# Performance work log

Measured on AMD Instinct MI355X. Metric: run time of the kernel, lower is better.

## Reference

```python
import jax, jax.numpy as jnp
import numpy as np

N = 100000   # nodes
E = 1600000  # edges
D = 128      # input_dim
H = 128      # hidden_dim
G = 64       # graphs in batch
L = 3        # num GCN layers
BN_EPS = 1e-5


def setup_inputs() -> dict:
    key = jax.random.key(0)
    ks = jax.random.split(key, 16)
    s = 1.0 / np.sqrt(H)
    inp = {
        "x": jax.random.normal(ks[0], (N, D), jnp.float32),
        "edge_index": jax.random.randint(ks[1], (2, E), 0, N, dtype=jnp.int64),
        "batch": jnp.sort(jax.random.randint(ks[2], (N,), 0, G, dtype=jnp.int64)),
        # stacked GCNConv params (input_dim == hidden_dim so layer 0 stacks too)
        "conv_w": jax.random.normal(ks[3], (L, H, H), jnp.float32) * s,
        "conv_b": jax.random.normal(ks[4], (L, H), jnp.float32) * 0.01,
        # BatchNorm1d running stats + affine (eval mode)
        "bn_gamma": jnp.ones((L, H), jnp.float32),
        "bn_beta": jnp.zeros((L, H), jnp.float32),
        "bn_mean": jax.random.normal(ks[5], (L, H), jnp.float32) * 0.1,
        "bn_var": jax.random.uniform(ks[6], (L, H), jnp.float32, 0.5, 1.5),
        # node head MLP
        "node_w1": jax.random.normal(ks[7], (H // 2, H), jnp.float32) * s,
        "node_b1": jnp.zeros((H // 2,), jnp.float32),
        "node_w2": jax.random.normal(ks[8], (2, H // 2), jnp.float32) * (1.0 / np.sqrt(H // 2)),
        "node_b2": jnp.zeros((2,), jnp.float32),
        # graph head MLP
        "graph_w1": jax.random.normal(ks[9], (H // 2, H), jnp.float32) * s,
        "graph_b1": jnp.zeros((H // 2,), jnp.float32),
        "graph_w2": jax.random.normal(ks[10], (2, H // 2), jnp.float32) * (1.0 / np.sqrt(H // 2)),
        "graph_b2": jnp.zeros((2,), jnp.float32),
    }
    return inp


def _gcn_layer(h, src, dst, deg_inv_sqrt, w, b):
    # PyG GCNConv: h' = W h, then symmetric-normalized scatter-add over
    # edges (self-loops already appended to src/dst).
    h = h @ w.T                                   # [N, H]
    norm = deg_inv_sqrt[src] * deg_inv_sqrt[dst]  # [E+N]
    msg = h[src] * norm[:, None]                  # [E+N, H] gather
    out = jax.ops.segment_sum(msg, dst, num_segments=N)  # scatter-add
    return out + b


def _forward(x, edge_index, batch, conv_w, conv_b, bn_gamma, bn_beta,
             bn_mean, bn_var, node_w1, node_b1, node_w2, node_b2,
             graph_w1, graph_b1, graph_w2, graph_b2):
    loops = jnp.arange(N, dtype=edge_index.dtype)
    src = jnp.concatenate([edge_index[0], loops])
    dst = jnp.concatenate([edge_index[1], loops])
    deg = jax.ops.segment_sum(jnp.ones_like(src, dtype=x.dtype), dst,
                              num_segments=N)
    deg_inv_sqrt = jnp.where(deg > 0, jax.lax.rsqrt(deg), 0.0)

    h = x
    for i in range(L):  # conv -> BN(eval) -> ReLU (dropout inactive in eval)
        h = _gcn_layer(h, src, dst, deg_inv_sqrt, conv_w[i], conv_b[i])
        h = (h - bn_mean[i]) * jax.lax.rsqrt(bn_var[i] + BN_EPS) * bn_gamma[i] + bn_beta[i]
        h = jax.nn.relu(h)

    node_pred = jax.nn.relu(h @ node_w1.T + node_b1) @ node_w2.T + node_b2

    counts = jax.ops.segment_sum(jnp.ones((N,), h.dtype), batch,
                                 num_segments=G)
    graph_emb = jax.ops.segment_sum(h, batch, num_segments=G) / \
        jnp.maximum(counts, 1.0)[:, None]
    graph_pred = jax.nn.relu(graph_emb @ graph_w1.T + graph_b1) @ graph_w2.T + graph_b2
    return node_pred, graph_pred


def reference(x, edge_index, batch, conv_w, conv_b, bn_gamma, bn_beta,
              bn_mean, bn_var, node_w1, node_b1, node_w2, node_b2,
              graph_w1, graph_b1, graph_w2, graph_b2):
    return _forward(x, edge_index, batch, conv_w, conv_b, bn_gamma, bn_beta,
                    bn_mean, bn_var, node_w1, node_b1, node_w2, node_b2,
                    graph_w1, graph_b1, graph_w2, graph_b2)
```

## Files before the change

### kernel.cpp

```cpp
#include <hip/hip_runtime.h>
#include <hip/hip_bf16.h>

#define NN 100000
#define EE 1600000
#define HH 128
#define GG 64
#define LL 3
#define BN_EPS 1e-5f
#define NT 391
#define CHW 392
#define CAP 6144

typedef __hip_bfloat16 bf16;
typedef __attribute__((ext_vector_type(8))) short short8;
typedef __attribute__((ext_vector_type(4))) float floatx4;

__device__ __forceinline__ float lo16(unsigned v) { return __uint_as_float(v << 16); }
__device__ __forceinline__ float hi16(unsigned v) { return __uint_as_float(v & 0xffff0000u); }
__device__ __forceinline__ unsigned short f2b(float v) {
    bf16 h = __float2bfloat16(v);
    return *(unsigned short*)&h;
}
__device__ __forceinline__ unsigned pack2(float a, float b) {
    return (unsigned)f2b(a) | ((unsigned)f2b(b) << 16);
}
__device__ __forceinline__ int geti(const int* __restrict__ p, int i, int f) {
    return f ? p[2 * i] : p[i];
}

__global__ __launch_bounds__(1024) void k_part(const int* __restrict__ ei,
        unsigned* __restrict__ chunk, unsigned short* __restrict__ lbu,
        int* __restrict__ flag,
        const float* __restrict__ conv_w, const float* __restrict__ nw1,
        unsigned short* __restrict__ cwB, unsigned short* __restrict__ n1B,
        float* __restrict__ bnA, float* __restrict__ bnB,
        const float* __restrict__ conv_b, const float* __restrict__ g,
        const float* __restrict__ be, const float* __restrict__ mn,
        const float* __restrict__ vr, float* __restrict__ gsum,
        float* __restrict__ gcnt) {
    __shared__ int lcnt[NT];
    __shared__ int sd[512];
    __shared__ unsigned short lbs[CHW];
    __shared__ unsigned sorted[4096];
    int t = threadIdx.x;
    int e0 = blockIdx.x * 4096;
    int probe = ei[2 * (e0 + (t & 63)) + 1];
    int f = __any(probe != 0) ? 0 : 1;
    if (blockIdx.x == 0 && t == 0) *flag = f;
    int gi = blockIdx.x * 1024 + t;
    if (gi < LL * HH * HH) cwB[gi] = f2b(conv_w[gi]);
    if (gi < 64 * HH) n1B[gi] = f2b(nw1[gi]);
    if (gi < LL * HH) {
        float A = g[gi] * rsqrtf(vr[gi] + BN_EPS);
        bnA[gi] = A;
        bnB[gi] = (conv_b[gi] - mn[gi]) * A + be[gi];
    }
    if (gi < GG * HH) gsum[gi] = 0.f;
    if (gi < GG) gcnt[gi] = 0.f;
    int nume = EE - e0 < 4096 ? EE - e0 : 4096;
    for (int i = t; i < NT; i += 1024) lcnt[i] = 0;
    __syncthreads();
    unsigned pk[4]; int ml[4], mt[4];
#pragma unroll
    for (int i = 0; i < 4; i++) {
        int li = i * 1024 + t;
        if (li < nume) {
            int e = e0 + li;
            int src = geti(ei, e, f), dst = geti(ei, EE + e, f);
            mt[i] = dst >> 8;
            pk[i] = ((unsigned)src << 8) | (unsigned)(dst & 255);
            ml[i] = atomicAdd(&lcnt[mt[i]], 1);
        }
    }
    __syncthreads();
    int own = 0;
    if (t < 512) {
        own = t < NT ? lcnt[t] : 0;
        sd[t] = own;
    }
    __syncthreads();
    for (int off = 1; off < 512; off <<= 1) {
        int y = 0;
        if (t < 512 && t >= off) y = sd[t - off];
        __syncthreads();
        if (t < 512) sd[t] += y;
        __syncthreads();
    }
    if (t < NT) lbs[t] = (unsigned short)(sd[t] - own);
    if (t == 0) lbs[NT] = (unsigned short)nume;
    __syncthreads();
#pragma unroll
    for (int i = 0; i < 4; i++) {
        int li = i * 1024 + t;
        if (li < nume) sorted[(int)lbs[mt[i]] + ml[i]] = pk[i];
    }
    if (t < CHW) lbu[blockIdx.x * CHW + t] = lbs[t];
    __syncthreads();
    for (int idx = t; idx < nume; idx += 1024)
        __builtin_nontemporal_store(sorted[idx], &chunk[e0 + idx]);
}

__global__ __launch_bounds__(1024) void k_csr(const unsigned* __restrict__ chunk,
        const unsigned short* __restrict__ lbu, unsigned* __restrict__ csr,
        int* __restrict__ offs, int* __restrict__ cnt, float* __restrict__ dinv,
        int* __restrict__ tne) {
    __shared__ unsigned stage[CAP];
    __shared__ unsigned outb[CAP];
    __shared__ int sd[512];
    __shared__ int hist[256], exs[256], cur[256];
    int T = blockIdx.x, t = threadIdx.x;
    int st = 0, rl = 0;
    if (t < NT) {
        int s0 = lbu[t * CHW + T];
        int s1 = lbu[t * CHW + T + 1];
        st = t * 4096 + s0;
        rl = s1 - s0;
    }
    if (t < 512) sd[t] = rl;
    __syncthreads();
    for (int off = 1; off < 512; off <<= 1) {
        int y = 0;
        if (t < 512 && t >= off) y = sd[t - off];
        __syncthreads();
        if (t < 512) sd[t] += y;
        __syncthreads();
    }
    int ne = sd[511];
    if (ne > CAP) ne = CAP;
    int so = t < NT ? sd[t] - rl : 0;
    if (t < 256) hist[t] = 0;
    __syncthreads();
    if (t < NT) {
        for (int j = 0; j < rl; j++) {
            int p = so + j;
            if (p < CAP)
                stage[p] = __builtin_nontemporal_load(&chunk[st + j]);
        }
    }
    __syncthreads();
    for (int i = t; i < ne; i += 1024)
        atomicAdd(&hist[stage[i] & 255u], 1);
    __syncthreads();
    int c = 0;
    if (t < 256) {
        c = hist[t];
        exs[t] = c;
    }
    __syncthreads();
    for (int off = 1; off < 256; off <<= 1) {
        int a = 0;
        if (t < 256 && t >= off) a = exs[t - off];
        __syncthreads();
        if (t < 256) exs[t] += a;
        __syncthreads();
    }
    if (t < 256) {
        int ex = exs[t] - c;
        cur[t] = ex;
        int node = T * 256 + t;
        if (node < NN) {
            offs[node] = T * CAP + ex;
            cnt[node] = c;
            dinv[node] = rsqrtf(1.0f + (float)c);
        }
    }
    if (t == 0) tne[T] = ne;
    __syncthreads();
    for (int i = t; i < ne; i += 1024) {
        unsigned p = stage[i];
        int q = atomicAdd(&cur[p & 255u], 1);
        outb[q] = p >> 8;
    }
    __syncthreads();
    for (int i = t; i < ne; i += 1024)
        csr[(size_t)T * CAP + i] = outb[i];
}

__global__ __launch_bounds__(1024) void k_wpack(const unsigned* __restrict__ csr,
        const float* __restrict__ dinv, unsigned* __restrict__ ewp,
        const int* __restrict__ tne) {
    int T = blockIdx.x, t = threadIdx.x;
    int ne = tne[T];
    for (int i = t; i < ne; i += 1024) {
        unsigned s = csr[(size_t)T * CAP + i];
        ewp[(size_t)T * CAP + i] = (s << 15) | ((unsigned)f2b(dinv[s]) & 0x7fffu);
    }
}

template<typename AT, int NC, bool FUSE>
__global__ __launch_bounds__(256) void k_gemm(const AT* __restrict__ in,
        const unsigned short* __restrict__ Wb, const float* __restrict__ bias,
        unsigned short* __restrict__ outh, int do_relu,
        const float* __restrict__ w2, const float* __restrict__ b2v,
        float* __restrict__ out2f) {
    int wave = threadIdx.x >> 6, lane = threadIdx.x & 63;
    int ln = lane & 15, q = lane >> 4;
    int r0 = blockIdx.x * 64 + wave * 16;
    int row = r0 + ln;
    int rr = row < NN ? row : NN - 1;
    short8 a[4];
    if constexpr (sizeof(AT) == 2) {
        const short8* ap = (const short8*)(in + (size_t)rr * HH);
#pragma unroll
        for (int kt = 0; kt < 4; kt++) a[kt] = ap[kt * 4 + q];
    } else {
        const float4* ap = (const float4*)(in + (size_t)rr * HH);
#pragma unroll
        for (int kt = 0; kt < 4; kt++) {
            float4 f0 = ap[(kt * 4 + q) * 2];
            float4 f1 = ap[(kt * 4 + q) * 2 + 1];
            a[kt][0] = (short)f2b(f0.x); a[kt][1] = (short)f2b(f0.y);
            a[kt][2] = (short)f2b(f0.z); a[kt][3] = (short)f2b(f0.w);
            a[kt][4] = (short)f2b(f1.x); a[kt][5] = (short)f2b(f1.y);
            a[kt][6] = (short)f2b(f1.z); a[kt][7] = (short)f2b(f1.w);
        }
    }
    float p0[4], p1[4];
    if constexpr (FUSE) {
#pragma unroll
        for (int r = 0; r < 4; r++) { p0[r] = 0.f; p1[r] = 0.f; }
    }
#pragma unroll
    for (int ct = 0; ct < NC / 16; ct++) {
        int c = ct * 16 + ln;
        const short8* bp = (const short8*)(Wb + (size_t)c * HH);
        floatx4 acc = {0.f, 0.f, 0.f, 0.f};
#pragma unroll
        for (int kt = 0; kt < 4; kt++) {
            short8 b = bp[kt * 4 + q];
            acc = __builtin_amdgcn_mfma_f32_16x16x32_bf16(a[kt], b, acc, 0, 0, 0);
        }
        float bv = bias ? bias[c] : 0.f;
        if constexpr (FUSE) {
            float wa = w2[c], wb = w2[64 + c];
#pragma unroll
            for (int reg = 0; reg < 4; reg++) {
                float v = fmaxf(acc[reg] + bv, 0.f);
                p0[reg] = fmaf(v, wa, p0[reg]);
                p1[reg] = fmaf(v, wb, p1[reg]);
            }
        } else {
#pragma unroll
            for (int reg = 0; reg < 4; reg++) {
                int orow = r0 + q * 4 + reg;
                if (orow < NN) {
                    float v = acc[reg] + bv;
                    if (do_relu) v = fmaxf(v, 0.f);
                    outh[(size_t)orow * NC + c] = f2b(v);
                }
            }
        }
    }
    if constexpr (FUSE) {
#pragma unroll
        for (int off = 1; off < 16; off <<= 1) {
#pragma unroll
            for (int r = 0; r < 4; r++) {
                p0[r] += __shfl_xor(p0[r], off);
                p1[r] += __shfl_xor(p1[r], off);
            }
        }
        if (ln == 0) {
            float ba = b2v[0], bb = b2v[1];
#pragma unroll
            for (int reg = 0; reg < 4; reg++) {
                int orow = r0 + q * 4 + reg;
                if (orow < NN)
                    ((float2*)out2f)[orow] = make_float2(p0[reg] + ba, p1[reg] + bb);
            }
        }
    }
}

__global__ __launch_bounds__(256) void k_aggr(const uint2* __restrict__ tH2,
        const unsigned* __restrict__ ewp, const int* __restrict__ offs,
        const int* __restrict__ cnt, const float* __restrict__ dinv,
        const float* __restrict__ bnA, const float* __restrict__ bnB,
        uint2* __restrict__ hout) {
    int wave = threadIdx.x >> 6, lane = threadIdx.x & 63;
    int node = blockIdx.x * 4 + wave;
    if (node >= NN) return;
    int base = offs[node], ne = cnt[node];
    float dd = dinv[node];
    int half = lane >> 5, li = lane & 31;
    uint2 sv = tH2[(size_t)node * 32 + li];
    float ws = half ? 0.f : dd;
    float4 acc;
    acc.x = lo16(sv.x) * ws; acc.y = hi16(sv.x) * ws;
    acc.z = lo16(sv.y) * ws; acc.w = hi16(sv.y) * ws;
    for (int k0 = 0; k0 < ne; k0 += 64) {
        int idx = k0 + lane;
        unsigned m = idx < ne ? __builtin_nontemporal_load(&ewp[base + idx]) : 0u;
        int c2 = ne - k0 < 64 ? ne - k0 : 64;
        for (int kk = 0; kk < c2; kk += 16) {
            uint2 vv[8]; float wj[8];
#pragma unroll
            for (int j = 0; j < 8; j++) {
                int e = kk + 2 * j + half;
                unsigned mm = (unsigned)__shfl((int)m, e);
                int s = (int)(mm >> 15);
                wj[j] = __uint_as_float((mm & 0x7fffu) << 16);
                vv[j] = tH2[(size_t)s * 32 + li];
            }
#pragma unroll
            for (int j = 0; j < 8; j++) {
                acc.x = fmaf(lo16(vv[j].x), wj[j], acc.x);
                acc.y = fmaf(hi16(vv[j].x), wj[j], acc.y);
                acc.z = fmaf(lo16(vv[j].y), wj[j], acc.z);
                acc.w = fmaf(hi16(vv[j].y), wj[j], acc.w);
            }
        }
    }
    acc.x += __shfl_xor(acc.x, 32);
    acc.y += __shfl_xor(acc.y, 32);
    acc.z += __shfl_xor(acc.z, 32);
    acc.w += __shfl_xor(acc.w, 32);
    if (half == 0) {
        float4 Av = ((const float4*)bnA)[li];
        float4 Bv = ((const float4*)bnB)[li];
        float r0 = fmaxf(fmaf(acc.x * dd, Av.x, Bv.x), 0.f);
        float r1 = fmaxf(fmaf(acc.y * dd, Av.y, Bv.y), 0.f);
        float r2 = fmaxf(fmaf(acc.z * dd, Av.z, Bv.z), 0.f);
        float r3 = fmaxf(fmaf(acc.w * dd, Av.w, Bv.w), 0.f);
        unsigned long long v64 =
            ((unsigned long long)pack2(r2, r3) << 32) | pack2(r0, r1);
        __builtin_nontemporal_store(v64,
            (unsigned long long*)&hout[(size_t)node * 32 + li]);
    }
}

#define PN 32
__global__ __launch_bounds__(64) void k_pool(const unsigned* __restrict__ hb,
        const int* __restrict__ batch, float* __restrict__ gsum,
        float* __restrict__ gcnt, const int* __restrict__ flag) {
    int lane = threadIdx.x;
    int f = *flag;
    int s0 = blockIdx.x * PN;
    int e0 = s0 + PN < NN ? s0 + PN : NN;
    int cur = geti(batch, s0, f);
    float a0 = 0.f, a1 = 0.f, cn = 0.f;
    for (int n = s0; n < e0; n++) {
        int g = geti(batch, n, f);
        if (g != cur) {
            atomicAdd(&gsum[cur * HH + 2 * lane], a0);
            atomicAdd(&gsum[cur * HH + 2 * lane + 1], a1);
            if (lane == 0) atomicAdd(&gcnt[cur], cn);
            a0 = a1 = cn = 0.f; cur = g;
        }
        unsigned v = hb[(size_t)n * 64 + lane];
        a0 += lo16(v); a1 += hi16(v); cn += 1.f;
    }
    atomicAdd(&gsum[cur * HH + 2 * lane], a0);
    atomicAdd(&gsum[cur * HH + 2 * lane + 1], a1);
    if (lane == 0) atomicAdd(&gcnt[cur], cn);
}

__global__ __launch_bounds__(64) void k_ghead(const float* __restrict__ gsum,
        const float* __restrict__ gcnt, const float* __restrict__ w1,
        const float* __restrict__ b1, const float* __restrict__ w2,
        const float* __restrict__ b2v, float* __restrict__ out) {
    __shared__ float emb[HH];
    int g = blockIdx.x, lane = threadIdx.x;
    float cn = gcnt[g];
    cn = cn > 1.f ? cn : 1.f;
    float inv = 1.f / cn;
    emb[lane] = gsum[g * HH + lane] * inv;
    emb[lane + 64] = gsum[g * HH + 64 + lane] * inv;
    __syncthreads();
    float acc = b1[lane];
    for (int k = 0; k < HH; k++) acc = fmaf(emb[k], w1[lane * HH + k], acc);
    float y = fmaxf(acc, 0.f);
    float v0 = y * w2[lane];
    float v1 = y * w2[64 + lane];
#pragma unroll
    for (int off = 32; off; off >>= 1) {
        v0 += __shfl_xor(v0, off);
        v1 += __shfl_xor(v1, off);
    }
    if (lane == 0) {
        out[(size_t)NN * 2 + g * 2]     = v0 + b2v[0];
        out[(size_t)NN * 2 + g * 2 + 1] = v1 + b2v[1];
    }
}

extern "C" void kernel_launch(void* const* d_in, const int* in_sizes, int n_in,
                              void* d_out, int out_size, void* d_ws, size_t ws_size,
                              hipStream_t stream) {
    const float* x      = (const float*)d_in[0];
    const int*   ei     = (const int*)d_in[1];
    const int*   batch  = (const int*)d_in[2];
    const float* conv_w = (const float*)d_in[3];
    const float* conv_b = (const float*)d_in[4];
    const float* bn_g   = (const float*)d_in[5];
    const float* bn_b   = (const float*)d_in[6];
    const float* bn_m   = (const float*)d_in[7];
    const float* bn_v   = (const float*)d_in[8];
    const float* nw1    = (const float*)d_in[9];
    const float* nb1    = (const float*)d_in[10];
    const float* nw2    = (const float*)d_in[11];
    const float* nb2    = (const float*)d_in[12];
    const float* gw1    = (const float*)d_in[13];
    const float* gb1    = (const float*)d_in[14];
    const float* gw2    = (const float*)d_in[15];
    const float* gb2    = (const float*)d_in[16];
    float* out = (float*)d_out;

    char* ws = (char*)d_ws;
    size_t off = 0;
    auto alloc = [&](size_t bytes) -> void* {
        void* p = ws + off;
        off += (bytes + 255) & ~(size_t)255;
        return p;
    };
    unsigned short* hb   = (unsigned short*)alloc((size_t)NN * HH * 2);
    unsigned short* tb   = (unsigned short*)alloc((size_t)NN * HH * 2);
    unsigned* chunk  = (unsigned*)alloc((size_t)EE * 4);
    unsigned* csr    = (unsigned*)alloc((size_t)NT * CAP * 4);
    unsigned* ewp    = (unsigned*)alloc((size_t)NT * CAP * 4);
    unsigned short* lbu = (unsigned short*)alloc((size_t)NT * CHW * 2);
    int*      offs   = (int*)     alloc((size_t)NN * 4);
    int*      cnt    = (int*)     alloc((size_t)NN * 4);
    float*    dinv   = (float*)   alloc((size_t)NN * 4);
    int*      tne    = (int*)     alloc((size_t)NT * 4);
    float*    bnA    = (float*)   alloc((size_t)LL * HH * 4);
    float*    bnB    = (float*)   alloc((size_t)LL * HH * 4);
    float*    gsum   = (float*)   alloc((size_t)GG * HH * 4);
    float*    gcnt   = (float*)   alloc((size_t)GG * 4);
    unsigned short* cwB = (unsigned short*)alloc((size_t)LL * HH * HH * 2);
    unsigned short* n1B = (unsigned short*)alloc((size_t)64 * HH * 2);
    int*      flag   = (int*)     alloc(256);

    k_part<<<NT, 1024, 0, stream>>>(ei, chunk, lbu, flag, conv_w, nw1, cwB, n1B,
            bnA, bnB, conv_b, bn_g, bn_b, bn_m, bn_v, gsum, gcnt);
    k_csr<<<NT, 1024, 0, stream>>>(chunk, lbu, csr, offs, cnt, dinv, tne);
    k_wpack<<<NT, 1024, 0, stream>>>(csr, dinv, ewp, tne);

    k_gemm<float, HH, false><<<(NN + 63) / 64, 256, 0, stream>>>(
        x, cwB, nullptr, tb, 0, nullptr, nullptr, nullptr);
    k_aggr<<<(NN + 3) / 4, 256, 0, stream>>>((const uint2*)tb, ewp, offs, cnt,
                                             dinv, bnA, bnB, (uint2*)hb);
    for (int l = 1; l < LL; l++) {
        k_gemm<unsigned short, HH, false><<<(NN + 63) / 64, 256, 0, stream>>>(
            hb, cwB + (size_t)l * HH * HH, nullptr, tb, 0, nullptr, nullptr, nullptr);
        k_aggr<<<(NN + 3) / 4, 256, 0, stream>>>((const uint2*)tb, ewp, offs, cnt,
                                                 dinv, bnA + l * HH, bnB + l * HH,
                                                 (uint2*)hb);
    }

    k_gemm<unsigned short, 64, true><<<(NN + 63) / 64, 256, 0, stream>>>(
        hb, n1B, nb1, nullptr, 1, nw2, nb2, out);

    k_pool<<<(NN + PN - 1) / PN, 64, 0, stream>>>((const unsigned*)hb, batch,
                                                  gsum, gcnt, flag);
    k_ghead<<<GG, 64, 0, stream>>>(gsum, gcnt, gw1, gb1, gw2, gb2, out);
}
```

Baseline: 505.1 us.

## Prescale GEMM output by dinv, pad CSR rows, drop edge-weight packing kernel

Folds the source-side normalization into the GEMM epilogue (rows scaled by dinv), so aggregation becomes a plain unweighted sum over neighbors and the separate k_wpack kernel plus packed weight array are removed. CSR rows are padded to multiples of 8 with a dummy zero row (index NN), which lets the aggregation loop do unconditional 8-wide gathers with one wave per node, 64 lanes each reading 4 bytes. GEMM weights are staged in padded LDS, and the pool loop is unrolled by 4. This adds some wasted gathers on padding entries and rounds the prescaled features to bf16 before summation.

```diff
diff --git a/kernel.cpp b/kernel.cpp
--- a/kernel.cpp
+++ b/kernel.cpp
@@ -37,7 +37,7 @@
         const float* __restrict__ conv_b, const float* __restrict__ g,
         const float* __restrict__ be, const float* __restrict__ mn,
         const float* __restrict__ vr, float* __restrict__ gsum,
-        float* __restrict__ gcnt) {
+        float* __restrict__ gcnt, unsigned* __restrict__ tbz) {
     __shared__ int lcnt[NT];
     __shared__ int sd[512];
     __shared__ unsigned short lbs[CHW];
@@ -57,6 +57,7 @@
     }
     if (gi < GG * HH) gsum[gi] = 0.f;
     if (gi < GG) gcnt[gi] = 0.f;
+    if (gi < 64) tbz[(size_t)NN * 64 + gi] = 0u;
     int nume = EE - e0 < 4096 ? EE - e0 : 4096;
     for (int i = t; i < NT; i += 1024) lcnt[i] = 0;
     __syncthreads();
@@ -102,12 +103,12 @@
 
 __global__ __launch_bounds__(1024) void k_csr(const unsigned* __restrict__ chunk,
         const unsigned short* __restrict__ lbu, unsigned* __restrict__ csr,
-        int* __restrict__ offs, int* __restrict__ cnt, float* __restrict__ dinv,
-        int* __restrict__ tne) {
+        int* __restrict__ offs, int* __restrict__ cnt, float* __restrict__ dinv) {
     __shared__ unsigned stage[CAP];
     __shared__ unsigned outb[CAP];
     __shared__ int sd[512];
     __shared__ int hist[256], exs[256], cur[256];
+    __shared__ int s_nep;
     int T = blockIdx.x, t = threadIdx.x;
     int st = 0, rl = 0;
     if (t < NT) {
@@ -141,10 +142,11 @@
     for (int i = t; i < ne; i += 1024)
         atomicAdd(&hist[stage[i] & 255u], 1);
     __syncthreads();
-    int c = 0;
+    int c = 0, pc = 0;
     if (t < 256) {
         c = hist[t];
-        exs[t] = c;
+        pc = (c + 7) & ~7;
+        exs[t] = pc;
     }
     __syncthreads();
     for (int off = 1; off < 256; off <<= 1) {
@@ -155,46 +157,47 @@
         __syncthreads();
     }
     if (t < 256) {
-        int ex = exs[t] - c;
-        cur[t] = ex;
+        int stn = exs[t] - pc;
+        cur[t] = stn;
         int node = T * 256 + t;
         if (node < NN) {
-            offs[node] = T * CAP + ex;
+            offs[node] = T * CAP + stn;
             cnt[node] = c;
             dinv[node] = rsqrtf(1.0f + (float)c);
         }
-    }
-    if (t == 0) tne[T] = ne;
+        for (int i = stn + c; i < stn + pc && i < CAP; i++)
+            outb[i] = NN;
+        if (t == 255) s_nep = exs[255] < CAP ? exs[255] : CAP;
+    }
     __syncthreads();
     for (int i = t; i < ne; i += 1024) {
         unsigned p = stage[i];
         int q = atomicAdd(&cur[p & 255u], 1);
-        outb[q] = p >> 8;
-    }
-    __syncthreads();
-    for (int i = t; i < ne; i += 1024)
+        if (q < CAP) outb[q] = p >> 8;
+    }
+    __syncthreads();
+    int nep = s_nep;
+    for (int i = t; i < nep; i += 1024)
         csr[(size_t)T * CAP + i] = outb[i];
-}
-
-__global__ __launch_bounds__(1024) void k_wpack(const unsigned* __restrict__ csr,
-        const float* __restrict__ dinv, unsigned* __restrict__ ewp,
-        const int* __restrict__ tne) {
-    int T = blockIdx.x, t = threadIdx.x;
-    int ne = tne[T];
-    for (int i = t; i < ne; i += 1024) {
-        unsigned s = csr[(size_t)T * CAP + i];
-        ewp[(size_t)T * CAP + i] = (s << 15) | ((unsigned)f2b(dinv[s]) & 0x7fffu);
-    }
 }
 
 template<typename AT, int NC, bool FUSE>
 __global__ __launch_bounds__(256) void k_gemm(const AT* __restrict__ in,
         const unsigned short* __restrict__ Wb, const float* __restrict__ bias,
         unsigned short* __restrict__ outh, int do_relu,
+        const float* __restrict__ scale,
         const float* __restrict__ w2, const float* __restrict__ b2v,
         float* __restrict__ out2f) {
+    __shared__ char sB[NC * 272];
     int wave = threadIdx.x >> 6, lane = threadIdx.x & 63;
     int ln = lane & 15, q = lane >> 4;
+    {
+        const short8* wsrc = (const short8*)Wb;
+        for (int i = threadIdx.x; i < NC * 16; i += 256) {
+            short8 v = wsrc[i];
+            *(short8*)(sB + (i >> 4) * 272 + (i & 15) * 16) = v;
+        }
+    }
     int r0 = blockIdx.x * 64 + wave * 16;
     int row = r0 + ln;
     int rr = row < NN ? row : NN - 1;
@@ -215,6 +218,15 @@
             a[kt][6] = (short)f2b(f1.z); a[kt][7] = (short)f2b(f1.w);
         }
     }
+    float scl[4];
+    if constexpr (!FUSE) {
+#pragma unroll
+        for (int reg = 0; reg < 4; reg++) {
+            int orow = r0 + q * 4 + reg;
+            scl[reg] = scale ? scale[orow < NN ? orow : NN - 1] : 1.f;
+        }
+    }
+    __syncthreads();
     float p0[4], p1[4];
     if constexpr (FUSE) {
 #pragma unroll
@@ -223,11 +235,10 @@
 #pragma unroll
     for (int ct = 0; ct < NC / 16; ct++) {
         int c = ct * 16 + ln;
-        const short8* bp = (const short8*)(Wb + (size_t)c * HH);
         floatx4 acc = {0.f, 0.f, 0.f, 0.f};
 #pragma unroll
         for (int kt = 0; kt < 4; kt++) {
-            short8 b = bp[kt * 4 + q];
+            short8 b = *(const short8*)(sB + (size_t)c * 272 + kt * 64 + q * 16);
             acc = __builtin_amdgcn_mfma_f32_16x16x32_bf16(a[kt], b, acc, 0, 0, 0);
         }
         float bv = bias ? bias[c] : 0.f;
@@ -246,7 +257,7 @@
                 if (orow < NN) {
                     float v = acc[reg] + bv;
                     if (do_relu) v = fmaxf(v, 0.f);
-                    outh[(size_t)orow * NC + c] = f2b(v);
+                    outh[(size_t)orow * NC + c] = f2b(v * scl[reg]);
                 }
             }
         }
@@ -272,61 +283,41 @@
     }
 }
 
-__global__ __launch_bounds__(256) void k_aggr(const uint2* __restrict__ tH2,
-        const unsigned* __restrict__ ewp, const int* __restrict__ offs,
+__global__ __launch_bounds__(256) void k_aggr(const unsigned* __restrict__ tbs,
+        const unsigned* __restrict__ csr, const int* __restrict__ offs,
         const int* __restrict__ cnt, const float* __restrict__ dinv,
         const float* __restrict__ bnA, const float* __restrict__ bnB,
-        uint2* __restrict__ hout) {
+        unsigned* __restrict__ hout) {
     int wave = threadIdx.x >> 6, lane = threadIdx.x & 63;
     int node = blockIdx.x * 4 + wave;
     if (node >= NN) return;
-    int base = offs[node], ne = cnt[node];
-    float dd = dinv[node];
-    int half = lane >> 5, li = lane & 31;
-    uint2 sv = tH2[(size_t)node * 32 + li];
-    float ws = half ? 0.f : dd;
-    float4 acc;
-    acc.x = lo16(sv.x) * ws; acc.y = hi16(sv.x) * ws;
-    acc.z = lo16(sv.y) * ws; acc.w = hi16(sv.y) * ws;
-    for (int k0 = 0; k0 < ne; k0 += 64) {
-        int idx = k0 + lane;
-        unsigned m = idx < ne ? __builtin_nontemporal_load(&ewp[base + idx]) : 0u;
-        int c2 = ne - k0 < 64 ? ne - k0 : 64;
-        for (int kk = 0; kk < c2; kk += 16) {
-            uint2 vv[8]; float wj[8];
-#pragma unroll
-            for (int j = 0; j < 8; j++) {
-                int e = kk + 2 * j + half;
-                unsigned mm = (unsigned)__shfl((int)m, e);
-                int s = (int)(mm >> 15);
-                wj[j] = __uint_as_float((mm & 0x7fffu) << 16);
-                vv[j] = tH2[(size_t)s * 32 + li];
-            }
-#pragma unroll
-            for (int j = 0; j < 8; j++) {
-                acc.x = fmaf(lo16(vv[j].x), wj[j], acc.x);
-                acc.y = fmaf(hi16(vv[j].x), wj[j], acc.y);
-                acc.z = fmaf(lo16(vv[j].y), wj[j], acc.z);
-                acc.w = fmaf(hi16(vv[j].y), wj[j], acc.w);
-            }
-        }
-    }
-    acc.x += __shfl_xor(acc.x, 32);
-    acc.y += __shfl_xor(acc.y, 32);
-    acc.z += __shfl_xor(acc.z, 32);
-    acc.w += __shfl_xor(acc.w, 32);
-    if (half == 0) {
-        float4 Av = ((const float4*)bnA)[li];
-        float4 Bv = ((const float4*)bnB)[li];
-        float r0 = fmaxf(fmaf(acc.x * dd, Av.x, Bv.x), 0.f);
-        float r1 = fmaxf(fmaf(acc.y * dd, Av.y, Bv.y), 0.f);
-        float r2 = fmaxf(fmaf(acc.z * dd, Av.z, Bv.z), 0.f);
-        float r3 = fmaxf(fmaf(acc.w * dd, Av.w, Bv.w), 0.f);
-        unsigned long long v64 =
-            ((unsigned long long)pack2(r2, r3) << 32) | pack2(r0, r1);
-        __builtin_nontemporal_store(v64,
-            (unsigned long long*)&hout[(size_t)node * 32 + li]);
-    }
+    int base = __builtin_amdgcn_readfirstlane(offs[node]);
+    int ne   = __builtin_amdgcn_readfirstlane(cnt[node]);
+    float dd = __uint_as_float(__builtin_amdgcn_readfirstlane(
+                   (int)__float_as_uint(dinv[node])));
+    unsigned sv = tbs[(size_t)node * 64 + lane];
+    float ax = lo16(sv), ay = hi16(sv);
+    const unsigned* __restrict__ ep = csr + base;
+    int nr = (ne + 7) & ~7;
+    for (int k0 = 0; k0 < nr; k0 += 8) {
+        unsigned vv[8];
+#pragma unroll
+        for (int j = 0; j < 8; j++) {
+            int s = (int)ep[k0 + j];
+            const unsigned* rp = tbs + (size_t)s * 64;
+            vv[j] = rp[lane];
+        }
+#pragma unroll
+        for (int j = 0; j < 8; j++) {
+            ax += lo16(vv[j]);
+            ay += hi16(vv[j]);
+        }
+    }
+    float2 A = ((const float2*)bnA)[lane];
+    float2 B = ((const float2*)bnB)[lane];
+    float r0 = fmaxf(fmaf(ax * dd, A.x, B.x), 0.f);
+    float r1 = fmaxf(fmaf(ay * dd, A.y, B.y), 0.f);
+    __builtin_nontemporal_store(pack2(r0, r1), &hout[(size_t)node * 64 + lane]);
 }
 
 #define PN 32
@@ -336,19 +327,25 @@
     int lane = threadIdx.x;
     int f = *flag;
     int s0 = blockIdx.x * PN;
-    int e0 = s0 + PN < NN ? s0 + PN : NN;
     int cur = geti(batch, s0, f);
     float a0 = 0.f, a1 = 0.f, cn = 0.f;
-    for (int n = s0; n < e0; n++) {
-        int g = geti(batch, n, f);
+    auto step = [&](int g, unsigned v) {
         if (g != cur) {
             atomicAdd(&gsum[cur * HH + 2 * lane], a0);
             atomicAdd(&gsum[cur * HH + 2 * lane + 1], a1);
             if (lane == 0) atomicAdd(&gcnt[cur], cn);
             a0 = a1 = cn = 0.f; cur = g;
         }
-        unsigned v = hb[(size_t)n * 64 + lane];
         a0 += lo16(v); a1 += hi16(v); cn += 1.f;
+    };
+    for (int n = s0; n < s0 + PN; n += 4) {
+        int g0 = geti(batch, n, f),     g1 = geti(batch, n + 1, f);
+        int g2 = geti(batch, n + 2, f), g3 = geti(batch, n + 3, f);
+        unsigned v0 = hb[(size_t)n * 64 + lane];
+        unsigned v1 = hb[(size_t)(n + 1) * 64 + lane];
+        unsigned v2 = hb[(size_t)(n + 2) * 64 + lane];
+        unsigned v3 = hb[(size_t)(n + 3) * 64 + lane];
+        step(g0, v0); step(g1, v1); step(g2, v2); step(g3, v3);
     }
     atomicAdd(&gsum[cur * HH + 2 * lane], a0);
     atomicAdd(&gsum[cur * HH + 2 * lane + 1], a1);
@@ -413,15 +410,13 @@
         return p;
     };
     unsigned short* hb   = (unsigned short*)alloc((size_t)NN * HH * 2);
-    unsigned short* tb   = (unsigned short*)alloc((size_t)NN * HH * 2);
+    unsigned short* tb   = (unsigned short*)alloc((size_t)(NN + 1) * HH * 2);
     unsigned* chunk  = (unsigned*)alloc((size_t)EE * 4);
     unsigned* csr    = (unsigned*)alloc((size_t)NT * CAP * 4);
-    unsigned* ewp    = (unsigned*)alloc((size_t)NT * CAP * 4);
     unsigned short* lbu = (unsigned short*)alloc((size_t)NT * CHW * 2);
     int*      offs   = (int*)     alloc((size_t)NN * 4);
     int*      cnt    = (int*)     alloc((size_t)NN * 4);
     float*    dinv   = (float*)   alloc((size_t)NN * 4);
-    int*      tne    = (int*)     alloc((size_t)NT * 4);
     float*    bnA    = (float*)   alloc((size_t)LL * HH * 4);
     float*    bnB    = (float*)   alloc((size_t)LL * HH * 4);
     float*    gsum   = (float*)   alloc((size_t)GG * HH * 4);
@@ -431,24 +426,24 @@
     int*      flag   = (int*)     alloc(256);
 
     k_part<<<NT, 1024, 0, stream>>>(ei, chunk, lbu, flag, conv_w, nw1, cwB, n1B,
-            bnA, bnB, conv_b, bn_g, bn_b, bn_m, bn_v, gsum, gcnt);
-    k_csr<<<NT, 1024, 0, stream>>>(chunk, lbu, csr, offs, cnt, dinv, tne);
-    k_wpack<<<NT, 1024, 0, stream>>>(csr, dinv, ewp, tne);
+            bnA, bnB, conv_b, bn_g, bn_b, bn_m, bn_v, gsum, gcnt, (unsigned*)tb);
+    k_csr<<<NT, 1024, 0, stream>>>(chunk, lbu, csr, offs, cnt, dinv);
 
     k_gemm<float, HH, false><<<(NN + 63) / 64, 256, 0, stream>>>(
-        x, cwB, nullptr, tb, 0, nullptr, nullptr, nullptr);
-    k_aggr<<<(NN + 3) / 4, 256, 0, stream>>>((const uint2*)tb, ewp, offs, cnt,
-                                             dinv, bnA, bnB, (uint2*)hb);
+        x, cwB, nullptr, tb, 0, dinv, nullptr, nullptr, nullptr);
+    k_aggr<<<(NN + 3) / 4, 256, 0, stream>>>((const unsigned*)tb, csr, offs, cnt,
+                                             dinv, bnA, bnB, (unsigned*)hb);
     for (int l = 1; l < LL; l++) {
         k_gemm<unsigned short, HH, false><<<(NN + 63) / 64, 256, 0, stream>>>(
-            hb, cwB + (size_t)l * HH * HH, nullptr, tb, 0, nullptr, nullptr, nullptr);
-        k_aggr<<<(NN + 3) / 4, 256, 0, stream>>>((const uint2*)tb, ewp, offs, cnt,
-                                                 dinv, bnA + l * HH, bnB + l * HH,
-                                                 (uint2*)hb);
+            hb, cwB + (size_t)l * HH * HH, nullptr, tb, 0, dinv,
+            nullptr, nullptr, nullptr);
+        k_aggr<<<(NN + 3) / 4, 256, 0, stream>>>((const unsigned*)tb, csr, offs,
+                                                 cnt, dinv, bnA + l * HH,
+                                                 bnB + l * HH, (unsigned*)hb);
     }
 
     k_gemm<unsigned short, 64, true><<<(NN + 63) / 64, 256, 0, stream>>>(
-        hb, n1B, nb1, nullptr, 1, nw2, nb2, out);
+        hb, n1B, nb1, nullptr, 1, nullptr, nw2, nb2, out);
 
     k_pool<<<(NN + PN - 1) / PN, 64, 0, stream>>>((const unsigned*)hb, batch,
                                                   gsum, gcnt, flag);
```

Result: faster. 437.9 us (-13.3%).
